# Kernel optimization log

Hardware: AMD Instinct MI355X
Metric: run time of the kernel (lower is better)

The kernel has to match this reference:

```python
import jax, jax.numpy as jnp
import numpy as np
import math

WINDOW_SIZE = 11
SIGMA = 1.5
C3 = 0.0001


def _make_window(window_size=WINDOW_SIZE, sigma=SIGMA):
    # 1D gaussian, normalized, then outer product -> [1,1,K,K] (OIHW)
    xs = np.arange(window_size, dtype=np.float64)
    g = np.exp(-((xs - window_size // 2) ** 2) / (2.0 * sigma ** 2))
    g = g / g.sum()
    w2d = np.outer(g, g).astype(np.float32)
    return jnp.asarray(w2d)[None, None, :, :]


def setup_inputs() -> dict:
    key = jax.random.key(0)
    k1, k2 = jax.random.split(key)
    B, C, H, W = 32, 1, 512, 512
    input1 = jax.random.normal(k1, (B, C, H, W), dtype=jnp.float32)
    input2 = jax.random.normal(k2, (B, C, H, W), dtype=jnp.float32)
    window = _make_window()
    return {"input1": input1, "input2": input2, "window": window}


def _conv_valid(x, window):
    # x: [N,1,H,W], window: [1,1,K,K], channel=1 so groups=1 is exact
    return jax.lax.conv_general_dilated(
        x, window, window_strides=(1, 1), padding="VALID",
        dimension_numbers=("NCHW", "OIHW", "NCHW"))


def reference(input1, input2, window):
    B = input1.shape[0]
    # Fuse the five gaussian box-filters into one conv over a stacked batch
    stacked = jnp.concatenate(
        [input1, input2, input1 * input1, input2 * input2, input1 * input2],
        axis=0)  # [5B,1,H,W]
    filt = _conv_valid(stacked, window)  # [5B,1,H',W']
    mu1, mu2, e11, e22, e12 = (filt[i * B:(i + 1) * B] for i in range(5))
    sigma1_sq = e11 - mu1 * mu1
    sigma2_sq = e22 - mu2 * mu2
    sigma12 = e12 - mu1 * mu2
    s = (sigma12 + C3) / (jnp.sqrt(jnp.abs(sigma1_sq)) * jnp.sqrt(jnp.abs(sigma2_sq)) + C3)
    return jnp.mean(s)
```

## Files before the change

### kernel.cpp

```cpp
#include <hip/hip_runtime.h>
#include <math.h>

#define KW 11
#define HALO 10
#define TY 32
#define BATCH 32
#define HH 512
#define WW 512
#define OH 502
#define OW 502
#define NSX 8
#define WPB 4
#define NBX 2
#define NBY 16
#define NWAVE (BATCH * NBY * NSX)
#define C3V 1.0e-4f
#define SW 80

typedef float v2f __attribute__((ext_vector_type(2)));

static __device__ __forceinline__ float rfl(float x) {
    return __int_as_float(__builtin_amdgcn_readfirstlane(__float_as_int(x)));
}

__global__ __launch_bounds__(256) void ssim_strip_kernel(
    const float* __restrict__ in1,
    const float* __restrict__ in2,
    const float* __restrict__ win,
    double* __restrict__ partials)
{
    __shared__ v2f sh[WPB][KW][SW];

    const int t = threadIdx.x;
    const int wid = t >> 6;
    const int lane = t & 63;
    const int strip = blockIdx.x * WPB + wid;
    const int x0 = strip * 64;
    const int y0 = blockIdx.y * TY;
    const int img = blockIdx.z;

    const int nx = min(64, OW - x0);
    const int ny = min(TY, OH - y0);

    v2f gp[6];
    {
        const float c = sqrtf(win[5 * KW + 5]);
        #pragma unroll
        for (int i = 0; i < 6; ++i) {
            const float w = rfl(win[i * KW + 5] / c);
            gp[i] = (v2f){w, w};
        }
    }
    #define GW(j) gp[(j) <= 5 ? (j) : 10 - (j)]

    const float maskf = (lane < nx) ? 1.f : 0.f;
    const bool stager = lane < 40;
    const int scol = min(x0 + 2 * lane, WW - 2);
    const float* b1 = in1 + (size_t)img * HH * WW;
    const float* b2 = in2 + (size_t)img * HH * WW;

    v2f* const mysh = &sh[wid][0][0];

    v2f vaA, vbA, vaB, vbB;

#define LOADR_A(q) { const int rq = min(y0 + (q), HH - 1);            \
    vaA = *(const v2f*)(b1 + (size_t)rq * WW + scol);                 \
    vbA = *(const v2f*)(b2 + (size_t)rq * WW + scol); }
#define LOADR_B(q) { const int rq = min(y0 + (q), HH - 1);            \
    vaB = *(const v2f*)(b1 + (size_t)rq * WW + scol);                 \
    vbB = *(const v2f*)(b2 + (size_t)rq * WW + scol); }
#define WRITES_A(slot) { if (stager)                                   \
    *(float4*)&mysh[(slot) * SW + 2 * lane] =                          \
        make_float4(vaA.x, vbA.x, vaA.y, vbA.y); }
#define WRITES_B(slot) { if (stager)                                   \
    *(float4*)&mysh[(slot) * SW + 2 * lane] =                          \
        make_float4(vaB.x, vbB.x, vaB.y, vbB.y); }
#define RDWIN(slot) { const v2f* rp = mysh + (slot) * SW + lane;       \
    _Pragma("unroll") for (int j = 0; j < KW; ++j) W[j] = rp[j]; }

    v2f accab[KW], accsq[KW];
    float acc4[KW];
    #pragma unroll
    for (int i = 0; i < KW; ++i) {
        accab[i] = (v2f){0.f, 0.f}; accsq[i] = (v2f){0.f, 0.f}; acc4[i] = 0.f;
    }

    v2f W[KW];
    double tsum = 0.0;

    LOADR_A(0);
    WRITES_A(0);
    RDWIN(0);
    LOADR_A(1);
    LOADR_B(2);

#define PHASE(p, S) {                                                   \
    const int yr = cbase + (p);                                         \
        \
    __builtin_amdgcn_s_setprio(1);                                      \
    v2f hab = (v2f){0.f, 0.f}, hsq = (v2f){0.f, 0.f};                   \
    float h4 = 0.f;                                                     \
    _Pragma("unroll")                                                   \
    for (int j = 0; j < KW; ++j) {                                      \
        const v2f ab = W[j];                                            \
        const v2f g = GW(j);                                            \
        const v2f gab = g * ab;                                         \
        hab = __builtin_elementwise_fma(g, ab, hab);                    \
        hsq = __builtin_elementwise_fma(gab, ab, hsq);                  \
        h4 = fmaf(gab.x, ab.y, h4);                                     \
    }                                                                   \
    __builtin_amdgcn_s_setprio(0);                                      \
             \
    WRITES_##S(((p) + 1) % KW);                                         \
                                \
    RDWIN(((p) + 1) % KW);                                              \
                                 \
    LOADR_##S(yr + 3);                                                  \
      \
                       \
    __builtin_amdgcn_s_setprio(1);                                      \
    _Pragma("unroll")                                                   \
    for (int r = 0; r < KW; ++r) {                                      \
        const int j = (r - (p) + KW) % KW;                              \
        const v2f g = GW(10 - j);                                       \
        if (j == 10) {                                                  \
            accab[r] = g * hab;                                         \
            accsq[r] = g * hsq;                                         \
            acc4[r] = g.x * h4;                                         \
        } else {                                                        \
            accab[r] = __builtin_elementwise_fma(g, hab, accab[r]);     \
            accsq[r] = __builtin_elementwise_fma(g, hsq, accsq[r]);     \
            acc4[r] = fmaf(g.x, h4, acc4[r]);                           \
        }                                                               \
    }                                                                   \
      \
    if (yr >= HALO) {                                                   \
        const v2f mu = accab[(p)];                                      \
        const v2f sq = __builtin_elementwise_fma(-mu, mu, accsq[(p)]);  \
        const float s12 = fmaf(-mu.x, mu.y, acc4[(p)]);                 \
        const float den = __builtin_amdgcn_sqrtf(fabsf(sq.x * sq.y)) + C3V; \
        const float s = (s12 + C3V) * __builtin_amdgcn_rcpf(den);       \
        const float m = ((yr - HALO) < ny) ? maskf : 0.f;               \
        csum = fmaf(s, m, csum);                                        \
    }                                                                   \
    __builtin_amdgcn_s_setprio(0);                                      \
}

    for (int c = 0; c < 4; ++c) {
        const int cbase = c * KW;
        float csum = 0.f;
        PHASE(0, A) PHASE(1, B) PHASE(2, A) PHASE(3, B) PHASE(4, A)
        PHASE(5, B) PHASE(6, A) PHASE(7, B) PHASE(8, A) PHASE(9, B)
        PHASE(10, A)
        tsum += (double)csum;
        { v2f tmp;
          tmp = vaA; vaA = vaB; vaB = tmp;
          tmp = vbA; vbA = vbB; vbB = tmp; }
    }
#undef PHASE
#undef LOADR_A
#undef LOADR_B
#undef WRITES_A
#undef WRITES_B
#undef RDWIN
#undef GW

    #pragma unroll
    for (int off = 32; off > 0; off >>= 1)
        tsum += __shfl_down(tsum, off, 64);
    if (lane == 0) {
        const int bid = (img * NBY + blockIdx.y) * NSX + strip;
        partials[bid] = tsum;
    }
}

__global__ __launch_bounds__(256) void ssim_reduce_kernel(
    const double* __restrict__ partials, float* __restrict__ out)
{
    __shared__ double sred[4];
    double s = 0.0;
    for (int i = threadIdx.x; i < NWAVE; i += 256) s += partials[i];
    #pragma unroll
    for (int off = 32; off > 0; off >>= 1)
        s += __shfl_down(s, off, 64);
    const int wid = threadIdx.x >> 6;
    const int lane = threadIdx.x & 63;
    if (lane == 0) sred[wid] = s;
    __syncthreads();
    if (threadIdx.x == 0) {
        const double total = sred[0] + sred[1] + sred[2] + sred[3];
        out[0] = (float)(total / ((double)BATCH * OH * OW));
    }
}

extern "C" void kernel_launch(void* const* d_in, const int* in_sizes, int n_in,
                              void* d_out, int out_size, void* d_ws, size_t ws_size,
                              hipStream_t stream) {
    const float* in1 = (const float*)d_in[0];
    const float* in2 = (const float*)d_in[1];
    const float* win = (const float*)d_in[2];
    float* out = (float*)d_out;
    double* partials = (double*)d_ws;

    dim3 grid(NBX, NBY, BATCH);
    dim3 block(WPB * 64);
    ssim_strip_kernel<<<grid, block, 0, stream>>>(in1, in2, win, partials);
    ssim_reduce_kernel<<<1, 256, 0, stream>>>(partials, out);
}
```

Baseline: 46.87 us.

## Process two rows per pipeline step in the sliding-window SSIM kernel

Restructures the per-row pipeline so each step handles two input rows: two window reads, two LDS writes and two global loads are issued together, followed by two horizontal convolutions and a fused vertical accumulation. The outer loop becomes two chunks of 22 rows instead of four chunks of 11. The aim is to batch memory operations and give more independent arithmetic between loads and their use, improving latency hiding. The cost is higher register pressure from the doubled window buffers and horizontal results, which could lower occupancy.

```diff
diff --git a/kernel.cpp b/kernel.cpp
--- a/kernel.cpp
+++ b/kernel.cpp
@@ -61,22 +61,22 @@
 
     v2f* const mysh = &sh[wid][0][0];
 
-    v2f vaA, vbA, vaB, vbB;
-
-#define LOADR_A(q) { const int rq = min(y0 + (q), HH - 1);            \
-    vaA = *(const v2f*)(b1 + (size_t)rq * WW + scol);                 \
-    vbA = *(const v2f*)(b2 + (size_t)rq * WW + scol); }
-#define LOADR_B(q) { const int rq = min(y0 + (q), HH - 1);            \
-    vaB = *(const v2f*)(b1 + (size_t)rq * WW + scol);                 \
-    vbB = *(const v2f*)(b2 + (size_t)rq * WW + scol); }
-#define WRITES_A(slot) { if (stager)                                   \
+    v2f va0, vb0, va1, vb1;
+
+#define LOADR0(q) { const int rq = min(y0 + (q), HH - 1);             \
+    va0 = *(const v2f*)(b1 + (size_t)rq * WW + scol);                 \
+    vb0 = *(const v2f*)(b2 + (size_t)rq * WW + scol); }
+#define LOADR1(q) { const int rq = min(y0 + (q), HH - 1);             \
+    va1 = *(const v2f*)(b1 + (size_t)rq * WW + scol);                 \
+    vb1 = *(const v2f*)(b2 + (size_t)rq * WW + scol); }
+#define WRITE0(slot) { if (stager)                                     \
     *(float4*)&mysh[(slot) * SW + 2 * lane] =                          \
-        make_float4(vaA.x, vbA.x, vaA.y, vbA.y); }
-#define WRITES_B(slot) { if (stager)                                   \
+        make_float4(va0.x, vb0.x, va0.y, vb0.y); }
+#define WRITE1(slot) { if (stager)                                     \
     *(float4*)&mysh[(slot) * SW + 2 * lane] =                          \
-        make_float4(vaB.x, vbB.x, vaB.y, vbB.y); }
-#define RDWIN(slot) { const v2f* rp = mysh + (slot) * SW + lane;       \
-    _Pragma("unroll") for (int j = 0; j < KW; ++j) W[j] = rp[j]; }
+        make_float4(va1.x, vb1.x, va1.y, vb1.y); }
+#define RDW(slot, Wa) { const v2f* rp = mysh + (slot) * SW + lane;     \
+    _Pragma("unroll") for (int j = 0; j < KW; ++j) Wa[j] = rp[j]; }
 
     v2f accab[KW], accsq[KW];
     float acc4[KW];
@@ -85,84 +85,101 @@
         accab[i] = (v2f){0.f, 0.f}; accsq[i] = (v2f){0.f, 0.f}; acc4[i] = 0.f;
     }
 
-    v2f W[KW];
+    v2f W0[KW], W1[KW];
     double tsum = 0.0;
 
-    LOADR_A(0);
-    WRITES_A(0);
-    RDWIN(0);
-    LOADR_A(1);
-    LOADR_B(2);
-
-#define PHASE(p, S) {                                                   \
-    const int yr = cbase + (p);                                         \
-        \
-    __builtin_amdgcn_s_setprio(1);                                      \
-    v2f hab = (v2f){0.f, 0.f}, hsq = (v2f){0.f, 0.f};                   \
-    float h4 = 0.f;                                                     \
+    LOADR0(0); LOADR1(1);
+    WRITE0(0); WRITE1(1);
+    LOADR0(2); LOADR1(3);
+
+#define HCONV(Wa, hab, hsq, h4) {                                       \
     _Pragma("unroll")                                                   \
     for (int j = 0; j < KW; ++j) {                                      \
-        const v2f ab = W[j];                                            \
+        const v2f ab = Wa[j];                                           \
         const v2f g = GW(j);                                            \
         const v2f gab = g * ab;                                         \
         hab = __builtin_elementwise_fma(g, ab, hab);                    \
         hsq = __builtin_elementwise_fma(gab, ab, hsq);                  \
         h4 = fmaf(gab.x, ab.y, h4);                                     \
+    } }
+
+#define EPI(r, orow) {                                                  \
+    const v2f mu = accab[r];                                            \
+    const v2f sq = __builtin_elementwise_fma(-mu, mu, accsq[r]);        \
+    const float s12 = fmaf(-mu.x, mu.y, acc4[r]);                       \
+    const float den = __builtin_amdgcn_sqrtf(fabsf(sq.x * sq.y)) + C3V; \
+    const float s = (s12 + C3V) * __builtin_amdgcn_rcpf(den);           \
+    const float m = ((orow) < ny) ? maskf : 0.f;                        \
+    csum = fmaf(s, m, csum);                                            \
+}
+
+#define PP(pp) {                                                        \
+    const int yr0 = cbase + 2 * (pp);                                   \
+                   \
+    RDW((2 * (pp)) % KW, W0);                                           \
+    RDW((2 * (pp) + 1) % KW, W1);                                       \
+                    \
+    WRITE0((2 * (pp) + 2) % KW);                                        \
+    WRITE1((2 * (pp) + 3) % KW);                                        \
+                     \
+    LOADR0(yr0 + 4);                                                    \
+    LOADR1(yr0 + 5);                                                    \
+    __builtin_amdgcn_s_setprio(1);                                      \
+          \
+    v2f habA = (v2f){0.f, 0.f}, hsqA = (v2f){0.f, 0.f};                 \
+    v2f habB = (v2f){0.f, 0.f}, hsqB = (v2f){0.f, 0.f};                 \
+    float h4A = 0.f, h4B = 0.f;                                         \
+    HCONV(W0, habA, hsqA, h4A);                                         \
+    HCONV(W1, habB, hsqB, h4B);                                         \
+            \
+    _Pragma("unroll")                                                   \
+    for (int r = 0; r < KW; ++r) {                                      \
+        const int je = (r - (2 * (pp)) % KW + KW) % KW;                 \
+                \
+        {                                                               \
+            const v2f g = GW(10 - je);                                  \
+            if (je == 10) {                                             \
+                accab[r] = g * habA; accsq[r] = g * hsqA;               \
+                acc4[r] = g.x * h4A;                                    \
+            } else {                                                    \
+                accab[r] = __builtin_elementwise_fma(g, habA, accab[r]); \
+                accsq[r] = __builtin_elementwise_fma(g, hsqA, accsq[r]); \
+                acc4[r] = fmaf(g.x, h4A, acc4[r]);                      \
+            }                                                           \
+        }                                                               \
+        if (je == 0) {                                                  \
+             \
+            if (yr0 >= HALO) EPI(r, yr0 - HALO);                        \
+            const v2f g = GW(0);                                        \
+            accab[r] = g * habB; accsq[r] = g * hsqB;                   \
+            acc4[r] = g.x * h4B;                                        \
+        } else {                                                        \
+            const int jo = je - 1;                                      \
+            const v2f g = GW(10 - jo);                                  \
+            accab[r] = __builtin_elementwise_fma(g, habB, accab[r]);    \
+            accsq[r] = __builtin_elementwise_fma(g, hsqB, accsq[r]);    \
+            acc4[r] = fmaf(g.x, h4B, acc4[r]);                          \
+            if (je == 1 && yr0 >= HALO) EPI(r, yr0 - HALO + 1);         \
+        }                                                               \
     }                                                                   \
     __builtin_amdgcn_s_setprio(0);                                      \
-             \
-    WRITES_##S(((p) + 1) % KW);                                         \
-                                \
-    RDWIN(((p) + 1) % KW);                                              \
-                                 \
-    LOADR_##S(yr + 3);                                                  \
-      \
-                       \
-    __builtin_amdgcn_s_setprio(1);                                      \
-    _Pragma("unroll")                                                   \
-    for (int r = 0; r < KW; ++r) {                                      \
-        const int j = (r - (p) + KW) % KW;                              \
-        const v2f g = GW(10 - j);                                       \
-        if (j == 10) {                                                  \
-            accab[r] = g * hab;                                         \
-            accsq[r] = g * hsq;                                         \
-            acc4[r] = g.x * h4;                                         \
-        } else {                                                        \
-            accab[r] = __builtin_elementwise_fma(g, hab, accab[r]);     \
-            accsq[r] = __builtin_elementwise_fma(g, hsq, accsq[r]);     \
-            acc4[r] = fmaf(g.x, h4, acc4[r]);                           \
-        }                                                               \
-    }                                                                   \
-      \
-    if (yr >= HALO) {                                                   \
-        const v2f mu = accab[(p)];                                      \
-        const v2f sq = __builtin_elementwise_fma(-mu, mu, accsq[(p)]);  \
-        const float s12 = fmaf(-mu.x, mu.y, acc4[(p)]);                 \
-        const float den = __builtin_amdgcn_sqrtf(fabsf(sq.x * sq.y)) + C3V; \
-        const float s = (s12 + C3V) * __builtin_amdgcn_rcpf(den);       \
-        const float m = ((yr - HALO) < ny) ? maskf : 0.f;               \
-        csum = fmaf(s, m, csum);                                        \
-    }                                                                   \
-    __builtin_amdgcn_s_setprio(0);                                      \
-}
-
-    for (int c = 0; c < 4; ++c) {
-        const int cbase = c * KW;
+}
+
+    for (int c = 0; c < 2; ++c) {
+        const int cbase = c * 22;
         float csum = 0.f;
-        PHASE(0, A) PHASE(1, B) PHASE(2, A) PHASE(3, B) PHASE(4, A)
-        PHASE(5, B) PHASE(6, A) PHASE(7, B) PHASE(8, A) PHASE(9, B)
-        PHASE(10, A)
+        PP(0) PP(1) PP(2) PP(3) PP(4) PP(5)
+        PP(6) PP(7) PP(8) PP(9) PP(10)
         tsum += (double)csum;
-        { v2f tmp;
-          tmp = vaA; vaA = vaB; vaB = tmp;
-          tmp = vbA; vbA = vbB; vbB = tmp; }
-    }
-#undef PHASE
-#undef LOADR_A
-#undef LOADR_B
-#undef WRITES_A
-#undef WRITES_B
-#undef RDWIN
+    }
+#undef PP
+#undef EPI
+#undef HCONV
+#undef LOADR0
+#undef LOADR1
+#undef WRITE0
+#undef WRITE1
+#undef RDW
 #undef GW
 
     #pragma unroll
```

Result: slower. 73.41 us (+56.6%).
